# Kernel optimization log

Hardware: AMD Instinct MI355X
Metric: run time of the kernel (lower is better)

## Reference

```python
import jax, jax.numpy as jnp
import numpy as np

B, C = 16384, 2048
DELTA_REL = 0.1


def setup_inputs() -> dict:
    key = jax.random.key(0)
    k1, k2, k3 = jax.random.split(key, 3)
    logits = jax.random.normal(k1, (B, C), dtype=jnp.float32)
    u = jax.random.uniform(k2, (B, C), dtype=jnp.float32)
    lab = (jax.random.uniform(k3, (B, C)) > 0.7).astype(jnp.float32)
    targets = jnp.where(u < 0.4, jnp.float32(jnp.nan), lab)
    return {"logits": logits, "targets": targets, "epoch": 3}


def _large_loss_rejection(logits, targets, epoch):
    unknown = jnp.isnan(targets)
    # unknown_to_negative: NaN -> 0 (negative label)
    t = jnp.where(unknown, 0.0, targets)
    # stable BCE-with-logits: softplus(x) - x*t
    losses = jax.nn.softplus(logits) - logits * t

    # --- no-grad mask construction ---
    ul = jax.lax.stop_gradient(losses) * unknown.astype(losses.dtype)
    percent = jnp.minimum(epoch * DELTA_REL, 1.0).astype(jnp.float32)
    n_unknown = jnp.count_nonzero(ul)
    k = jnp.round(n_unknown.astype(jnp.float32) * percent).astype(jnp.int32)
    k = jnp.maximum(k, 1)
    # k-th largest value of flattened unknown losses = topk(k).values.min()
    sorted_desc = jnp.sort(ul.reshape(-1))[::-1]
    loss_threshold = jax.lax.dynamic_slice(sorted_desc, (k - 1,), (1,))[0]
    lambdas = jnp.where(ul > loss_threshold, 0.0, 1.0)

    return losses * lambdas  # reduction='none'


def reference(logits, targets, epoch):
    return _large_loss_rejection(logits, targets, epoch)
```

## Files before the change

### kernel.cpp

```cpp
#include <hip/hip_runtime.h>
#include <math.h>

typedef float    f32x4 __attribute__((ext_vector_type(4)));
typedef unsigned u32x4 __attribute__((ext_vector_type(4)));

#define HC_OFF     0u
#define H12_OFF    16384u
#define H64_OFF    20480u
#define CTRL_OFF   20544u
#define ZERO_WORDS 20560u
#define CAND_OFF   20560u
#define CAND_CAP   900000u
#define LBUF       2048u

#define FLOOR_BITS 0x36000000u


__device__ __forceinline__ float softplus_exact(float x) {
    float ax = fabsf(x);
    float e = (float)exp(-(double)ax);
    float l = (float)log1p((double)e);
    return fmaxf(x, 0.0f) + l;
}
__device__ __forceinline__ unsigned exact_bits(float x) {
    return __float_as_uint(softplus_exact(x));
}

__device__ __forceinline__ unsigned refine_core(float x, float ax, float e,
                                                float sp) {
    unsigned cb = __float_as_uint(sp);
    float mf = 64.0f + 8.0f * ax;
    if (x < 0.0f) mf += __builtin_amdgcn_rcpf(e);
    bool need = (cb < FLOOR_BITS) || (mf >= 524288.0f);
    if (!need) {
        unsigned m = (unsigned)mf;
        unsigned low = cb & 0xFFFFFu;
        need = (low < m) || (low >= 0x100000u - m);
    }
    if (need) cb = exact_bits(x);
    return cb;
}
__device__ __forceinline__ unsigned refine_A(float x) {
    float ax = fabsf(x);
    float e = __expf(-ax);
    float sp = fmaxf(x, 0.0f) + __logf(1.0f + e);
    return refine_core(x, ax, e, sp);
}

__device__ __forceinline__ unsigned kA_elem(float x, float t,
                                            unsigned* __restrict__ sh) {
    float ax = fabsf(x);
    float e = __expf(-ax);
    float sp = fmaxf(x, 0.0f) + __logf(1.0f + e);
    unsigned outb;
    if (isnan(t)) {
        unsigned cb = refine_core(x, ax, e, sp) | 1u;
        if (cb != 1u) atomicAdd(&sh[cb >> 20], 1u);
        outb = cb;
    } else {
        float loss = sp - x * t;
        outb = __float_as_uint(loss) & ~1u;
    }
    return outb;
}

__global__ __launch_bounds__(256) void kA_store_hist(
    const float* __restrict__ lg, const float* __restrict__ tg,
    float* __restrict__ out, unsigned* __restrict__ ws, long long n) {
    __shared__ unsigned sh[4096];
    for (int i = threadIdx.x; i < 4096; i += 256) sh[i] = 0;
    __syncthreads();

    long long n8 = n >> 3;
    long long tid = (long long)blockIdx.x * 256 + threadIdx.x;
    long long stride = (long long)gridDim.x * 256;
    const f32x4* lg4 = (const f32x4*)lg;
    const f32x4* tg4 = (const f32x4*)tg;
    f32x4* out4 = (f32x4*)out;

    if (n8 % stride == 0) {
        long long iters = n8 / stride;
        f32x4 xa0, xb0, ta0, tb0, xa1, xb1, ta1, tb1;
        {
            long long i = tid;
            xa0 = lg4[2 * i]; xb0 = lg4[2 * i + 1];
            ta0 = __builtin_nontemporal_load(&tg4[2 * i]);
            tb0 = __builtin_nontemporal_load(&tg4[2 * i + 1]);
        }
        if (iters > 1) {
            long long i = tid + stride;
            xa1 = lg4[2 * i]; xb1 = lg4[2 * i + 1];
            ta1 = __builtin_nontemporal_load(&tg4[2 * i]);
            tb1 = __builtin_nontemporal_load(&tg4[2 * i + 1]);
        }
        for (long long it = 0; it < iters; ++it) {
            f32x4 pa, pb, pta, ptb;
            if (it + 2 < iters) {
                long long i = tid + (it + 2) * stride;
                pa = lg4[2 * i]; pb = lg4[2 * i + 1];
                pta = __builtin_nontemporal_load(&tg4[2 * i]);
                ptb = __builtin_nontemporal_load(&tg4[2 * i + 1]);
            }
            long long i = tid + it * stride;
            f32x4 oa, ob_;
            oa.x = __uint_as_float(kA_elem(xa0.x, ta0.x, sh));
            oa.y = __uint_as_float(kA_elem(xa0.y, ta0.y, sh));
            oa.z = __uint_as_float(kA_elem(xa0.z, ta0.z, sh));
            oa.w = __uint_as_float(kA_elem(xa0.w, ta0.w, sh));
            ob_.x = __uint_as_float(kA_elem(xb0.x, tb0.x, sh));
            ob_.y = __uint_as_float(kA_elem(xb0.y, tb0.y, sh));
            ob_.z = __uint_as_float(kA_elem(xb0.z, tb0.z, sh));
            ob_.w = __uint_as_float(kA_elem(xb0.w, tb0.w, sh));
            out4[2 * i] = oa;
            out4[2 * i + 1] = ob_;
            xa0 = xa1; xb0 = xb1; ta0 = ta1; tb0 = tb1;
            xa1 = pa; xb1 = pb; ta1 = pta; tb1 = ptb;
        }
    } else {
        for (long long i = tid; i < n8; i += stride) {
            f32x4 xa = lg4[2 * i], xb = lg4[2 * i + 1];
            f32x4 ta = tg4[2 * i], tb = tg4[2 * i + 1];
            f32x4 oa, ob_;
            oa.x = __uint_as_float(kA_elem(xa.x, ta.x, sh));
            oa.y = __uint_as_float(kA_elem(xa.y, ta.y, sh));
            oa.z = __uint_as_float(kA_elem(xa.z, ta.z, sh));
            oa.w = __uint_as_float(kA_elem(xa.w, ta.w, sh));
            ob_.x = __uint_as_float(kA_elem(xb.x, tb.x, sh));
            ob_.y = __uint_as_float(kA_elem(xb.y, tb.y, sh));
            ob_.z = __uint_as_float(kA_elem(xb.z, tb.z, sh));
            ob_.w = __uint_as_float(kA_elem(xb.w, tb.w, sh));
            out4[2 * i] = oa;
            out4[2 * i + 1] = ob_;
        }
    }
    if (tid == 0) {
        for (long long q = (n >> 3) << 3; q < n; ++q)
            out[q] = __uint_as_float(kA_elem(lg[q], tg[q], sh));
    }
    __syncthreads();
    unsigned* hist12 = ws + H12_OFF;
    for (int q = threadIdx.x; q < 4096; q += 256)
        if (sh[q]) atomicAdd(&hist12[q], sh[q]);
}

__global__ __launch_bounds__(256) void k2_sel12(
    unsigned* __restrict__ ws, const int* __restrict__ epoch_ptr) {
    const unsigned* hist12 = ws + H12_OFF;
    unsigned* ctrl = ws + CTRL_OFF;
    __shared__ unsigned long long chunk[256];
    int t = threadIdx.x;
    unsigned long long s = 0;
    for (int j = 0; j < 16; ++j) s += hist12[t * 16 + j];
    chunk[t] = s;
    __syncthreads();
    if (t == 0) {
        unsigned long long tot = 0;
        for (int c = 0; c < 256; ++c) tot += chunk[c];
        int epoch = epoch_ptr[0];
        float percent = fminf((float)epoch * 0.1f, 1.0f);
        float nf = (float)tot;
        float kr = rintf(nf * percent);
        long long k = (long long)kr;
        if (k < 1) k = 1;

        long long cum = 0;
        int b = -1;
        long long kprime = 0;
        for (int c = 255; c >= 0; --c) {
            if (cum + (long long)chunk[c] >= k) {
                long long cc = cum;
                for (int j = 15; j >= 0; --j) {
                    unsigned v = hist12[c * 16 + j];
                    if (cc + (long long)v >= k) {
                        b = c * 16 + j;
                        kprime = k - cc;
                        break;
                    }
                    cc += v;
                }
                break;
            }
            cum += chunk[c];
        }
        ctrl[0] = (unsigned)b;
        ctrl[1] = (unsigned)kprime;
        if (b < 0) {
            ctrl[2] = 0u;
            ctrl[4] = 0xFFFFFFFFu;
            ctrl[6] = 0u;
        } else {
            unsigned lo12 = (unsigned)b << 20;
            double vlo = (double)__uint_as_float(lo12);
            double vhi = (double)__uint_as_float(lo12 + 0xFFFFFu);
            double mb = 1e9;
            if (vlo > 1e-30) {
                double xlo = vlo + log1p(-exp(-vlo)) - 0.001;
                double xhi = vhi + log1p(-exp(-vhi)) + 0.001;
                double axmax = fmax(fabs(xlo), fabs(xhi));
                mb = 64.0 + 8.0 * ceil(axmax);
                if (xlo < 0.0) mb += exp(fmin(-xlo, 30.0));
                mb *= 2.0;
            }
            ctrl[6] = (mb >= 8192.0) ? 8192u : (unsigned)mb;
        }
    }
}

__global__ __launch_bounds__(256) void kB_hist64(
    const float* __restrict__ lg, const unsigned* __restrict__ ob,
    unsigned* __restrict__ ws, long long n) {
    unsigned b12 = ws[CTRL_OFF + 0];
    if (b12 == 0xFFFFFFFFu) return;
    unsigned lo12 = b12 << 20;
    unsigned hi12 = lo12 + (1u << 20);
    unsigned medge = ws[CTRL_OFF + 6] + 2u;

    __shared__ unsigned sh[64];
    __shared__ float buf[LBUF];
    __shared__ unsigned lcnt, gbase;
    if (threadIdx.x < 64) sh[threadIdx.x] = 0;
    if (threadIdx.x == 0) lcnt = 0;
    __syncthreads();

    float* cand = (float*)(ws + CAND_OFF);
    unsigned* cnt = ws + CTRL_OFF + 3;

    long long n4 = n >> 2;
    long long tid = (long long)blockIdx.x * 256 + threadIdx.x;
    long long stride = (long long)gridDim.x * 256;
    const u32x4* o4 = (const u32x4*)ob;

    long long i = tid;
    u32x4 u4;
    if (i < n4) u4 = o4[i];
    while (i < n4) {
        long long j = i + stride;
        u32x4 nu4;
        if (j < n4) nu4 = o4[j];
        unsigned us[4] = {u4.x, u4.y, u4.z, u4.w};
#pragma unroll
        for (int c = 0; c < 4; ++c) {
            unsigned u = us[c];
            if ((u & 1u) && u != 1u && u >= lo12 && u < hi12) {
                float x = lg[i * 4 + c];
                unsigned rB = u;
                unsigned d = u & 16383u;
                if (d < medge || d >= 16384u - medge)
                    rB = exact_bits(x) | 1u;
                atomicAdd(&sh[(rB >> 14) & 63u], 1u);
                unsigned li = atomicAdd(&lcnt, 1u);
                if (li < LBUF) buf[li] = x;
            }
        }
        u4 = nu4;
        i = j;
    }
    if (tid == 0) {
        for (long long q = (n4 << 2); q < n; ++q) {
            unsigned u = ob[q];
            if ((u & 1u) && u != 1u && u >= lo12 && u < hi12) {
                float x = lg[q];
                unsigned rB = u;
                unsigned d = u & 16383u;
                if (d < medge || d >= 16384u - medge) rB = exact_bits(x) | 1u;
                atomicAdd(&sh[(rB >> 14) & 63u], 1u);
                unsigned idx = atomicAdd(cnt, 1u);
                if (idx < CAND_CAP) cand[idx] = x;
            }
        }
    }
    __syncthreads();
    if (threadIdx.x < 64 && sh[threadIdx.x])
        atomicAdd(&ws[H64_OFF + threadIdx.x], sh[threadIdx.x]);
    if (threadIdx.x == 0) {
        unsigned add = (lcnt > LBUF) ? (CAND_CAP + 1u) : lcnt;
        gbase = atomicAdd(cnt, add);
    }
    __syncthreads();
    unsigned c2 = lcnt < LBUF ? lcnt : LBUF;
    for (unsigned q = threadIdx.x; q < c2; q += 256) {
        unsigned gi = gbase + q;
        if (gi < CAND_CAP) cand[gi] = buf[q];
    }
}

__global__ void k4_sel64(unsigned* __restrict__ ws) {
    unsigned* ctrl = ws + CTRL_OFF;
    if (ctrl[0] == 0xFFFFFFFFu) return;
    if (threadIdx.x == 0) {
        long long kprime = (long long)ctrl[1];
        long long cum = 0;
        int s = 0;
        long long kpp = 1;
        for (int j = 63; j >= 0; --j) {
            unsigned v = ws[H64_OFF + j];
            if (cum + (long long)v >= kprime) {
                s = j;
                kpp = kprime - cum;
                break;
            }
            cum += v;
        }
        ctrl[4] = (ctrl[0] << 20) + ((unsigned)s << 14);
        ctrl[5] = (unsigned)kpp;
    }
}

__global__ __launch_bounds__(256) void kC_histwin(
    const float* __restrict__ lg, const unsigned* __restrict__ ob,
    unsigned* __restrict__ ws, long long n) {
    unsigned wlo = ws[CTRL_OFF + 4];
    if (wlo == 0xFFFFFFFFu) return;
    unsigned whi = wlo + 16384u;
    unsigned medge = ws[CTRL_OFF + 6] + 2u;
    unsigned b12 = ws[CTRL_OFF + 0];
    unsigned lo12 = b12 << 20;
    unsigned hi12 = lo12 + (1u << 20);
    unsigned glo = (wlo - lo12 > medge) ? wlo - medge : lo12;
    unsigned ghi = (hi12 - whi > medge) ? whi + medge : hi12;
    unsigned count = ws[CTRL_OFF + 3];

    long long tid = (long long)blockIdx.x * 256 + threadIdx.x;
    long long stride = (long long)gridDim.x * 256;

    if (count <= CAND_CAP) {
        const float* cand = (const float*)(ws + CAND_OFF);
        for (long long i = tid; i < (long long)count; i += stride) {
            float x = cand[i];
            unsigned u = refine_A(x) | 1u;
            if (u >= glo && u < ghi) {
                unsigned eb = exact_bits(x);
                unsigned rB = u;
                unsigned d = u & 16383u;
                if (d < medge || d >= 16384u - medge) rB = eb | 1u;
                if (rB >= wlo && rB < whi) {
                    unsigned off = eb - wlo;
                    if (off < 16384u) atomicAdd(&ws[HC_OFF + off], 1u);
                }
            }
        }
    } else {
        long long n4 = n >> 2;
        const u32x4* o4 = (const u32x4*)ob;
        for (long long i = tid; i < n4; i += stride) {
            u32x4 u4 = o4[i];
            unsigned us[4] = {u4.x, u4.y, u4.z, u4.w};
#pragma unroll
            for (int c = 0; c < 4; ++c) {
                unsigned u = us[c];
                if ((u & 1u) && u != 1u && u >= glo && u < ghi) {
                    float x = lg[i * 4 + c];
                    unsigned eb = exact_bits(x);
                    unsigned rB = u;
                    unsigned d = u & 16383u;
                    if (d < medge || d >= 16384u - medge) rB = eb | 1u;
                    if (rB >= wlo && rB < whi) {
                        unsigned off = eb - wlo;
                        if (off < 16384u) atomicAdd(&ws[HC_OFF + off], 1u);
                    }
                }
            }
        }
        if (tid == 0) {
            for (long long q = (n4 << 2); q < n; ++q) {
                unsigned u = ob[q];
                if ((u & 1u) && u != 1u && u >= glo && u < ghi) {
                    unsigned eb = exact_bits(lg[q]);
                    unsigned rB = u;
                    unsigned d = u & 16383u;
                    if (d < medge || d >= 16384u - medge) rB = eb | 1u;
                    if (rB >= wlo && rB < whi) {
                        unsigned off = eb - wlo;
                        if (off < 16384u) atomicAdd(&ws[HC_OFF + off], 1u);
                    }
                }
            }
        }
    }
}

__global__ __launch_bounds__(1024) void k6_selwin(unsigned* __restrict__ ws) {
    unsigned* ctrl = ws + CTRL_OFF;
    if (ctrl[4] == 0xFFFFFFFFu) return;
    __shared__ unsigned long long csum[1024];
    int t = threadIdx.x;
    unsigned long long s = 0;
    for (int j = 0; j < 16; ++j) s += ws[HC_OFF + t * 16 + j];
    csum[t] = s;
    __syncthreads();
    if (t == 0) {
        long long kpp = (long long)ctrl[5];
        long long cum = 0;
        int sel = 0;
        long long rem = kpp;
        for (int c = 1023; c >= 0; --c) {
            if (cum + (long long)csum[c] >= kpp) {
                sel = c;
                rem = kpp - cum;
                break;
            }
            cum += csum[c];
        }
        long long cc = 0;
        int bsel = 0;
        for (int j = 15; j >= 0; --j) {
            unsigned v = ws[HC_OFF + sel * 16 + j];
            if (cc + (long long)v >= rem) {
                bsel = j;
                break;
            }
            cc += v;
        }
        ctrl[2] = ctrl[4] + (unsigned)(sel * 16 + bsel);
    }
}

__device__ __forceinline__ unsigned kD_elem(unsigned u, unsigned thr,
                                            unsigned mband,
                                            const float* __restrict__ lg,
                                            long long idx, bool* changed) {
    if (!(u & 1u)) return u;
    unsigned udiff = (u > thr) ? u - thr : thr - u;
    if (udiff <= mband) {
        unsigned eb = exact_bits(lg[idx]);
        unsigned r = (eb > thr) ? 0u : eb;
        *changed |= (r != u);
        return r;
    }
    if (u > thr) { *changed = true; return 0u; }
    return u;
}

__global__ __launch_bounds__(256) void kD_final(
    const float* __restrict__ lg, unsigned* __restrict__ ob,
    const unsigned* __restrict__ ws, long long n) {
    unsigned thr = ws[CTRL_OFF + 2];
    unsigned mband = ws[CTRL_OFF + 6] + 2u;

    long long n8 = n >> 3;
    long long tid = (long long)blockIdx.x * 256 + threadIdx.x;
    long long stride = (long long)gridDim.x * 256;
    u32x4* o4 = (u32x4*)ob;

    long long i = tid;
    u32x4 ua, ub;
    if (i < n8) {
        ua = o4[2 * i];
        ub = o4[2 * i + 1];
    }
    while (i < n8) {
        long long j = i + stride;
        u32x4 nua, nub;
        if (j < n8) {
            nua = o4[2 * j];
            nub = o4[2 * j + 1];
        }
        uint4_t: ;
        u32x4 va, vb;
        bool chA = false, chB = false;
        long long base = i * 8;
        va.x = kD_elem(ua.x, thr, mband, lg, base + 0, &chA);
        va.y = kD_elem(ua.y, thr, mband, lg, base + 1, &chA);
        va.z = kD_elem(ua.z, thr, mband, lg, base + 2, &chA);
        va.w = kD_elem(ua.w, thr, mband, lg, base + 3, &chA);
        vb.x = kD_elem(ub.x, thr, mband, lg, base + 4, &chB);
        vb.y = kD_elem(ub.y, thr, mband, lg, base + 5, &chB);
        vb.z = kD_elem(ub.z, thr, mband, lg, base + 6, &chB);
        vb.w = kD_elem(ub.w, thr, mband, lg, base + 7, &chB);
        if (chA) o4[2 * i] = va;
        if (chB) o4[2 * i + 1] = vb;
        ua = nua; ub = nub;
        i = j;
    }
    if (tid == 0) {
        for (long long q = (n >> 3) << 3; q < n; ++q) {
            bool ch = false;
            unsigned r = kD_elem(ob[q], thr, mband, lg, q, &ch);
            if (ch) ob[q] = r;
        }
    }
}

extern "C" void kernel_launch(void* const* d_in, const int* in_sizes, int n_in,
                              void* d_out, int out_size, void* d_ws, size_t ws_size,
                              hipStream_t stream) {
    const float* lg = (const float*)d_in[0];
    const float* tg = (const float*)d_in[1];
    const int* epoch = (const int*)d_in[2];
    float* out = (float*)d_out;
    unsigned* ob = (unsigned*)d_out;
    unsigned* ws = (unsigned*)d_ws;
    long long n = (long long)in_sizes[0];

    (void)hipMemsetAsync(d_ws, 0, (size_t)ZERO_WORDS * 4, stream);

    const int blocks = 2048, threads = 256;
    kA_store_hist<<<blocks, threads, 0, stream>>>(lg, tg, out, ws, n);
    k2_sel12<<<1, 256, 0, stream>>>(ws, epoch);
    kB_hist64<<<blocks, threads, 0, stream>>>(lg, ob, ws, n);
    k4_sel64<<<1, 64, 0, stream>>>(ws);
    kC_histwin<<<1024, threads, 0, stream>>>(lg, ob, ws, n);
    k6_selwin<<<1, 1024, 0, stream>>>(ws);
    kD_final<<<blocks, threads, 0, stream>>>(lg, ob, ws, n);
}
```

Baseline: 245.0 us.

## Zero above-bucket elements early and finalize only candidate indices

Result: faster. 216.9 us (-11.5%).

```diff
diff --git a/kernel.cpp b/kernel.cpp
--- a/kernel.cpp
+++ b/kernel.cpp
@@ -206,29 +206,29 @@
     }
 }
 
-__global__ __launch_bounds__(256) void kB_hist64(
-    const float* __restrict__ lg, const unsigned* __restrict__ ob,
+__global__ __launch_bounds__(256) void kB_zero(
+    const float* __restrict__ lg, unsigned* __restrict__ ob,
     unsigned* __restrict__ ws, long long n) {
     unsigned b12 = ws[CTRL_OFF + 0];
     if (b12 == 0xFFFFFFFFu) return;
     unsigned lo12 = b12 << 20;
-    unsigned hi12 = lo12 + (1u << 20);
+    unsigned hi12 = (b12 >= 4095u) ? 0xFFFFFFFFu : (lo12 + (1u << 20));
     unsigned medge = ws[CTRL_OFF + 6] + 2u;
 
     __shared__ unsigned sh[64];
-    __shared__ float buf[LBUF];
+    __shared__ unsigned buf[LBUF];
     __shared__ unsigned lcnt, gbase;
     if (threadIdx.x < 64) sh[threadIdx.x] = 0;
     if (threadIdx.x == 0) lcnt = 0;
     __syncthreads();
 
-    float* cand = (float*)(ws + CAND_OFF);
+    unsigned* cand = ws + CAND_OFF;
     unsigned* cnt = ws + CTRL_OFF + 3;
 
     long long n4 = n >> 2;
     long long tid = (long long)blockIdx.x * 256 + threadIdx.x;
     long long stride = (long long)gridDim.x * 256;
-    const u32x4* o4 = (const u32x4*)ob;
+    u32x4* o4 = (u32x4*)ob;
 
     long long i = tid;
     u32x4 u4;
@@ -241,15 +241,18 @@
 #pragma unroll
         for (int c = 0; c < 4; ++c) {
             unsigned u = us[c];
-            if ((u & 1u) && u != 1u && u >= lo12 && u < hi12) {
-                float x = lg[i * 4 + c];
-                unsigned rB = u;
-                unsigned d = u & 16383u;
-                if (d < medge || d >= 16384u - medge)
-                    rB = exact_bits(x) | 1u;
-                atomicAdd(&sh[(rB >> 14) & 63u], 1u);
-                unsigned li = atomicAdd(&lcnt, 1u);
-                if (li < LBUF) buf[li] = x;
+            if ((u & 1u) && u != 1u) {
+                if (u >= hi12) {
+                    ob[i * 4 + c] = 0u;
+                } else if (u >= lo12) {
+                    unsigned rB = u;
+                    unsigned d = u & 16383u;
+                    if (d < medge || d >= 16384u - medge)
+                        rB = exact_bits(lg[i * 4 + c]) | 1u;
+                    atomicAdd(&sh[(rB >> 14) & 63u], 1u);
+                    unsigned li = atomicAdd(&lcnt, 1u);
+                    if (li < LBUF) buf[li] = (unsigned)(i * 4 + c);
+                }
             }
         }
         u4 = nu4;
@@ -258,14 +261,18 @@
     if (tid == 0) {
         for (long long q = (n4 << 2); q < n; ++q) {
             unsigned u = ob[q];
-            if ((u & 1u) && u != 1u && u >= lo12 && u < hi12) {
-                float x = lg[q];
-                unsigned rB = u;
-                unsigned d = u & 16383u;
-                if (d < medge || d >= 16384u - medge) rB = exact_bits(x) | 1u;
-                atomicAdd(&sh[(rB >> 14) & 63u], 1u);
-                unsigned idx = atomicAdd(cnt, 1u);
-                if (idx < CAND_CAP) cand[idx] = x;
+            if ((u & 1u) && u != 1u) {
+                if (u >= hi12) {
+                    ob[q] = 0u;
+                } else if (u >= lo12) {
+                    unsigned rB = u;
+                    unsigned d = u & 16383u;
+                    if (d < medge || d >= 16384u - medge)
+                        rB = exact_bits(lg[q]) | 1u;
+                    atomicAdd(&sh[(rB >> 14) & 63u], 1u);
+                    unsigned idx = atomicAdd(cnt, 1u);
+                    if (idx < CAND_CAP) cand[idx] = (unsigned)q;
+                }
             }
         }
     }
@@ -315,7 +322,7 @@
     unsigned medge = ws[CTRL_OFF + 6] + 2u;
     unsigned b12 = ws[CTRL_OFF + 0];
     unsigned lo12 = b12 << 20;
-    unsigned hi12 = lo12 + (1u << 20);
+    unsigned hi12 = (b12 >= 4095u) ? 0xFFFFFFFFu : (lo12 + (1u << 20));
     unsigned glo = (wlo - lo12 > medge) ? wlo - medge : lo12;
     unsigned ghi = (hi12 - whi > medge) ? whi + medge : hi12;
     unsigned count = ws[CTRL_OFF + 3];
@@ -324,9 +331,10 @@
     long long stride = (long long)gridDim.x * 256;
 
     if (count <= CAND_CAP) {
-        const float* cand = (const float*)(ws + CAND_OFF);
+        const unsigned* cand = ws + CAND_OFF;
         for (long long i = tid; i < (long long)count; i += stride) {
-            float x = cand[i];
+            unsigned idx = cand[i];
+            float x = lg[idx];
             unsigned u = refine_A(x) | 1u;
             if (u >= glo && u < ghi) {
                 unsigned eb = exact_bits(x);
@@ -415,6 +423,30 @@
     }
 }
 
+__global__ __launch_bounds__(256) void kD_cand(
+    const float* __restrict__ lg, unsigned* __restrict__ ob,
+    const unsigned* __restrict__ ws) {
+    unsigned count = ws[CTRL_OFF + 3];
+    if (count > CAND_CAP) return;
+    unsigned thr = ws[CTRL_OFF + 2];
+    unsigned mband = ws[CTRL_OFF + 6] + 2u;
+    const unsigned* cand = ws + CAND_OFF;
+
+    long long tid = (long long)blockIdx.x * 256 + threadIdx.x;
+    long long stride = (long long)gridDim.x * 256;
+    for (long long i = tid; i < (long long)count; i += stride) {
+        unsigned idx = cand[i];
+        unsigned u = ob[idx];
+        unsigned udiff = (u > thr) ? u - thr : thr - u;
+        if (udiff <= mband) {
+            unsigned eb = exact_bits(lg[idx]);
+            if (eb > thr) ob[idx] = 0u;
+        } else if (u > thr) {
+            ob[idx] = 0u;
+        }
+    }
+}
+
 __device__ __forceinline__ unsigned kD_elem(unsigned u, unsigned thr,
                                             unsigned mband,
                                             const float* __restrict__ lg,
@@ -431,9 +463,10 @@
     return u;
 }
 
-__global__ __launch_bounds__(256) void kD_final(
+__global__ __launch_bounds__(256) void kD_full(
     const float* __restrict__ lg, unsigned* __restrict__ ob,
     const unsigned* __restrict__ ws, long long n) {
+    if (ws[CTRL_OFF + 3] <= CAND_CAP) return;
     unsigned thr = ws[CTRL_OFF + 2];
     unsigned mband = ws[CTRL_OFF + 6] + 2u;
 
@@ -442,20 +475,9 @@
     long long stride = (long long)gridDim.x * 256;
     u32x4* o4 = (u32x4*)ob;
 
-    long long i = tid;
-    u32x4 ua, ub;
-    if (i < n8) {
-        ua = o4[2 * i];
-        ub = o4[2 * i + 1];
-    }
-    while (i < n8) {
-        long long j = i + stride;
-        u32x4 nua, nub;
-        if (j < n8) {
-            nua = o4[2 * j];
-            nub = o4[2 * j + 1];
-        }
-        uint4_t: ;
+    for (long long i = tid; i < n8; i += stride) {
+        u32x4 ua = o4[2 * i];
+        u32x4 ub = o4[2 * i + 1];
         u32x4 va, vb;
         bool chA = false, chB = false;
         long long base = i * 8;
@@ -469,8 +491,6 @@
         vb.w = kD_elem(ub.w, thr, mband, lg, base + 7, &chB);
         if (chA) o4[2 * i] = va;
         if (chB) o4[2 * i + 1] = vb;
-        ua = nua; ub = nub;
-        i = j;
     }
     if (tid == 0) {
         for (long long q = (n >> 3) << 3; q < n; ++q) {
@@ -497,9 +517,10 @@
     const int blocks = 2048, threads = 256;
     kA_store_hist<<<blocks, threads, 0, stream>>>(lg, tg, out, ws, n);
     k2_sel12<<<1, 256, 0, stream>>>(ws, epoch);
-    kB_hist64<<<blocks, threads, 0, stream>>>(lg, ob, ws, n);
+    kB_zero<<<blocks, threads, 0, stream>>>(lg, ob, ws, n);
     k4_sel64<<<1, 64, 0, stream>>>(ws);
     kC_histwin<<<1024, threads, 0, stream>>>(lg, ob, ws, n);
     k6_selwin<<<1, 1024, 0, stream>>>(ws);
-    kD_final<<<blocks, threads, 0, stream>>>(lg, ob, ws, n);
-}
+    kD_cand<<<256, threads, 0, stream>>>(lg, ob, ws);
+    kD_full<<<blocks, threads, 0, stream>>>(lg, ob, ws, n);
+}
```
